# Kernel optimization log

Measured on AMD Instinct MI355X. Metric: run time of the kernel, lower is better.

Reference implementation:

```python
import jax, jax.numpy as jnp
import numpy as np

HEADS = 8
DIM_HEAD = 64
MAX_POS = 512
SCALE = DIM_HEAD ** -0.5

def setup_inputs() -> dict:
    key = jax.random.key(0)
    ks = jax.random.split(key, 4)
    b, n, dim = 32, 512, 512
    x = jax.random.normal(ks[0], (b, n, dim), dtype=jnp.float32)
    W_qkv = jax.random.normal(ks[1], (dim, 3 * HEADS * DIM_HEAD), dtype=jnp.float32) * (dim ** -0.5)
    rel_table = jax.random.normal(ks[2], (2 * MAX_POS + 1, DIM_HEAD), dtype=jnp.float32) * 0.02
    W_out = jax.random.normal(ks[3], (HEADS * DIM_HEAD, dim), dtype=jnp.float32) * ((HEADS * DIM_HEAD) ** -0.5)
    b_out = jnp.zeros((dim,), dtype=jnp.float32)
    return {"x": x, "W_qkv": W_qkv, "rel_table": rel_table, "W_out": W_out, "b_out": b_out}

def reference(x, W_qkv, rel_table, W_out, b_out):
    b, n, dim = x.shape
    qkv = x @ W_qkv  # [b, n, 3*h*d]
    q, k, v = jnp.split(qkv, 3, axis=-1)
    def heads(t):  # [b, n, h*d] -> [b, h, n, d]
        return t.reshape(b, n, HEADS, DIM_HEAD).transpose(0, 2, 1, 3)
    q, k, v = heads(q), heads(k), heads(v)
    dots = jnp.einsum('bhid,bhjd->bhij', q, k) * SCALE
    # relative position bias
    seq = jnp.arange(n)
    dist = jnp.clip(seq[:, None] - seq[None, :], -MAX_POS, MAX_POS) + MAX_POS  # [n, n]
    rel = rel_table[dist]  # [n, n(=r), d]
    pos_attn = jnp.einsum('bhnd,nrd->bhnr', q, rel) * SCALE
    dots = dots + pos_attn
    attn = jax.nn.softmax(dots.astype(jnp.float32), axis=-1).astype(q.dtype)
    out = jnp.einsum('bhij,bhjd->bhid', attn, v)  # [b, h, n, d]
    out = out.transpose(0, 2, 1, 3).reshape(b, n, HEADS * DIM_HEAD)
    return out @ W_out + b_out  # dropout=0.0 -> identity
```

## Files before the change

kernel.cpp:

```cpp
#include <hip/hip_runtime.h>

typedef __attribute__((ext_vector_type(8))) short short8;
typedef __attribute__((ext_vector_type(4))) float floatx4;

static constexpr size_t QOFF = 0;
static constexpr size_t KOFF = 8388608;
static constexpr size_t VTOFF = 16777216;
static constexpr size_t RBOFF = 25165824;
static constexpr size_t XBOFF = 25231424;
static constexpr size_t WTOFF = 33620032;
static constexpr size_t WOTOFF = 34406464;
static constexpr size_t OBOFF = 34668608;

__device__ inline unsigned short f2b(float f) {
  unsigned int u = __float_as_uint(f);
  u += 0x7fffu + ((u >> 16) & 1u);
  return (unsigned short)(u >> 16);
}
__device__ inline float b2f(unsigned short h) {
  return __uint_as_float(((unsigned int)h) << 16);
}

__global__ __launch_bounds__(256) void prep(const float* __restrict__ x,
                                            const float* __restrict__ Wqkv,
                                            const float* __restrict__ Wout,
                                            const float* __restrict__ rel,
                                            unsigned short* __restrict__ wsb) {
  __shared__ float T[64 * 65];
  const int bx = blockIdx.x;
  const int tid = threadIdx.x;
  if (bx < 4096) {
    size_t i8 = ((size_t)bx * 256 + tid) * 8;
    float4 a = *(const float4*)(x + i8);
    float4 b = *(const float4*)(x + i8 + 4);
    unsigned short t[8] = {f2b(a.x), f2b(a.y), f2b(a.z), f2b(a.w),
                           f2b(b.x), f2b(b.y), f2b(b.z), f2b(b.w)};
    *(uint4*)(wsb + XBOFF + i8) = *(uint4*)t;
  } else if (bx < 4352) {
    const bool isq = bx < 4288;
    const int z = isq ? bx - 4096 : bx - 4288;
    const int C = isq ? 1536 : 512;
    const int R = 512;
    const int c0 = (isq ? (z % 24) : (z % 8)) * 64;
    const int r0 = (isq ? (z / 24) : (z / 8)) * 64;
    const float* in = isq ? Wqkv : Wout;
    unsigned short* out = wsb + (isq ? WTOFF : WOTOFF);
#pragma unroll
    for (int p = 0; p < 4; ++p) {
      int r = (tid >> 4) + p * 16, c4 = (tid & 15) * 4;
      float4 v = *(const float4*)(in + (size_t)(r0 + r) * C + c0 + c4);
      T[r * 65 + c4 + 0] = v.x;
      T[r * 65 + c4 + 1] = v.y;
      T[r * 65 + c4 + 2] = v.z;
      T[r * 65 + c4 + 3] = v.w;
    }
    __syncthreads();
#pragma unroll
    for (int p = 0; p < 4; ++p) {
      int oc = (tid >> 4) + p * 16;
      int or4 = (tid & 15) * 4;
      unsigned short t[4];
#pragma unroll
      for (int j = 0; j < 4; ++j) t[j] = f2b(T[(or4 + j) * 65 + oc]);
      *(uint2*)(out + (size_t)(c0 + oc) * R + r0 + or4) = *(uint2*)t;
    }
  } else {
    int i = (bx - 4352) * 256 + tid;
    if (i < 65600) wsb[RBOFF + i] = f2b(rel[i]);
  }
}

__global__ __launch_bounds__(256) void qkv_mfma(const unsigned short* __restrict__ Xb,
                                                const unsigned short* __restrict__ Wt,
                                                unsigned short* __restrict__ wsb) {
  __shared__ __align__(16) unsigned short As[128 * 40];
  __shared__ __align__(16) unsigned short Bs[128 * 40];
  const int tid = threadIdx.x;
  const int w = tid >> 6, lane = tid & 63;
  const int g = lane >> 4, c = lane & 15;
  const int m0 = blockIdx.x * 128, n0 = blockIdx.y * 128;
  const int wr = (w >> 1) * 64, wc = (w & 1) * 64;
  const bool vmode = (blockIdx.y >= 8);

  const int rA = tid >> 2, oA = tid & 3;

  floatx4 acc[4][4];
#pragma unroll
  for (int mi = 0; mi < 4; ++mi)
#pragma unroll
    for (int ni = 0; ni < 4; ++ni) acc[mi][ni] = (floatx4){0.f, 0.f, 0.f, 0.f};

  uint4 pa0 = *(const uint4*)(Xb + (size_t)(m0 + rA) * 512 + oA * 8);
  uint4 pa1 = *(const uint4*)(Xb + (size_t)(m0 + rA + 64) * 512 + oA * 8);
  uint4 pb0 = *(const uint4*)(Wt + (size_t)(n0 + rA) * 512 + oA * 8);
  uint4 pb1 = *(const uint4*)(Wt + (size_t)(n0 + rA + 64) * 512 + oA * 8);

  for (int kk = 0; kk < 512; kk += 32) {
    __syncthreads();
    *(uint4*)(As + rA * 40 + oA * 8) = pa0;
    *(uint4*)(As + (rA + 64) * 40 + oA * 8) = pa1;
    *(uint4*)(Bs + rA * 40 + oA * 8) = pb0;
    *(uint4*)(Bs + (rA + 64) * 40 + oA * 8) = pb1;
    __syncthreads();
    const int kkn = (kk < 480) ? kk + 32 : kk;
    pa0 = *(const uint4*)(Xb + (size_t)(m0 + rA) * 512 + kkn + oA * 8);
    pa1 = *(const uint4*)(Xb + (size_t)(m0 + rA + 64) * 512 + kkn + oA * 8);
    pb0 = *(const uint4*)(Wt + (size_t)(n0 + rA) * 512 + kkn + oA * 8);
    pb1 = *(const uint4*)(Wt + (size_t)(n0 + rA + 64) * 512 + kkn + oA * 8);

    short8 a[4], b[4];
#pragma unroll
    for (int mi = 0; mi < 4; ++mi) a[mi] = *(const short8*)(As + (wr + mi * 16 + c) * 40 + g * 8);
#pragma unroll
    for (int ni = 0; ni < 4; ++ni) b[ni] = *(const short8*)(Bs + (wc + ni * 16 + c) * 40 + g * 8);
    if (vmode) {
#pragma unroll
      for (int mi = 0; mi < 4; ++mi)
#pragma unroll
        for (int ni = 0; ni < 4; ++ni)
          acc[mi][ni] = __builtin_amdgcn_mfma_f32_16x16x32_bf16(b[ni], a[mi], acc[mi][ni], 0, 0, 0);
    } else {
#pragma unroll
      for (int mi = 0; mi < 4; ++mi)
#pragma unroll
        for (int ni = 0; ni < 4; ++ni)
          acc[mi][ni] = __builtin_amdgcn_mfma_f32_16x16x32_bf16(a[mi], b[ni], acc[mi][ni], 0, 0, 0);
    }
  }

  constexpr float SCL = 0.125f * 1.44269504088896340736f;
  if (vmode) {
#pragma unroll
    for (int mi = 0; mi < 4; ++mi) {
      const int xrow = m0 + wr + mi * 16 + c;
      const int bb = xrow >> 9, nn = xrow & 511;
#pragma unroll
      for (int ni = 0; ni < 4; ++ni) {
#pragma unroll
        for (int r = 0; r < 4; ++r) {
          const int C = n0 + wc + ni * 16 + g * 4 + r;
          const int col512 = C & 511;
          const int h = col512 >> 6, d = col512 & 63;
          wsb[VTOFF + (size_t)(bb * 8 + h) * 32768 + (size_t)d * 512 + nn] = f2b(acc[mi][ni][r]);
        }
      }
    }
  } else {
    const size_t base = (blockIdx.y >= 4) ? KOFF : QOFF;
    const float scl = (blockIdx.y >= 4) ? 1.0f : SCL;
#pragma unroll
    for (int ni = 0; ni < 4; ++ni) {
      const int C = n0 + wc + ni * 16 + c;
      const int col512 = C & 511;
      const int h = col512 >> 6, d = col512 & 63;
#pragma unroll
      for (int mi = 0; mi < 4; ++mi) {
#pragma unroll
        for (int r = 0; r < 4; ++r) {
          const int xrow = m0 + wr + mi * 16 + g * 4 + r;
          wsb[base + (size_t)((xrow >> 9) * 8 + h) * 32768 + (size_t)(xrow & 511) * 64 + d] =
              f2b(acc[mi][ni][r] * scl);
        }
      }
    }
  }
}

__global__ __launch_bounds__(256) void attn_mfma(const unsigned short* __restrict__ wsb,
                                                 unsigned short* __restrict__ Ob) {
  __shared__ __align__(16) unsigned short Ks[64 * 72];
  __shared__ __align__(16) unsigned short Vt[64 * 72];
  __shared__ __align__(16) unsigned short Ps[64 * 72];
  __shared__ __align__(16) unsigned short Gs[4 * 16 * 84];

  const int tid = threadIdx.x;
  const int w = tid >> 6, lane = tid & 63;
  const int g = lane >> 4, c = lane & 15;
  const int i0 = blockIdx.x * 64, bh = blockIdx.y;

  const unsigned short* Qg = wsb + QOFF + (size_t)bh * 32768 + (size_t)i0 * 64;
  const unsigned short* Kg = wsb + KOFF + (size_t)bh * 32768;
  const unsigned short* Vg = wsb + VTOFF + (size_t)bh * 32768;
  const unsigned short* Rg = wsb + RBOFF;

  const short8 bq0 = *(const short8*)(Qg + (size_t)(w * 16 + c) * 64 + g * 8);
  const short8 bq1 = *(const short8*)(Qg + (size_t)(w * 16 + c) * 64 + 32 + g * 8);

  unsigned short* GsW = Gs + w * (16 * 84);
  unsigned short* PsW = Ps + (w * 16 + c) * 72;

  const int r0s = tid >> 3, o0s = tid & 7;
  const int r1s = r0s + 32;

  uint4 pk0 = *(const uint4*)(Kg + (size_t)r0s * 64 + o0s * 8);
  uint4 pk1 = *(const uint4*)(Kg + (size_t)r1s * 64 + o0s * 8);
  uint4 pv0 = *(const uint4*)(Vg + (size_t)r0s * 512 + o0s * 8);
  uint4 pv1 = *(const uint4*)(Vg + (size_t)r1s * 512 + o0s * 8);

  float m_i = -1e30f, l_i = 0.f;
  floatx4 oa[4];
#pragma unroll
  for (int t = 0; t < 4; ++t) oa[t] = (floatx4){0.f, 0.f, 0.f, 0.f};

  for (int jc = 0; jc < 8; ++jc) {
    const int j0 = jc * 64;
    __syncthreads();
    *(uint4*)(Ks + r0s * 72 + o0s * 8) = pk0;
    *(uint4*)(Ks + r1s * 72 + o0s * 8) = pk1;
    *(uint4*)(Vt + r0s * 72 + o0s * 8) = pv0;
    *(uint4*)(Vt + r1s * 72 + o0s * 8) = pv1;
    __syncthreads();

    const int dbase = i0 - j0 + 449 + w * 16;
    const unsigned short* Trow = Rg + (size_t)(dbase + c) * 64;
    short8 t0[5], t1[5];
#pragma unroll
    for (int dd = 0; dd < 5; ++dd) {
      t0[dd] = *(const short8*)(Trow + dd * 1024 + g * 8);
      t1[dd] = *(const short8*)(Trow + dd * 1024 + 32 + g * 8);
    }
    const int j0n = (jc < 7) ? j0 + 64 : j0;
    pk0 = *(const uint4*)(Kg + (size_t)(j0n + r0s) * 64 + o0s * 8);
    pk1 = *(const uint4*)(Kg + (size_t)(j0n + r1s) * 64 + o0s * 8);
    pv0 = *(const uint4*)(Vg + (size_t)r0s * 512 + j0n + o0s * 8);
    pv1 = *(const uint4*)(Vg + (size_t)r1s * 512 + j0n + o0s * 8);

    floatx4 s4[4];
#pragma unroll
    for (int t = 0; t < 4; ++t) {
      short8 k0 = *(const short8*)(Ks + (t * 16 + c) * 72 + g * 8);
      short8 k1 = *(const short8*)(Ks + (t * 16 + c) * 72 + 32 + g * 8);
      floatx4 sa = (floatx4){0.f, 0.f, 0.f, 0.f};
      sa = __builtin_amdgcn_mfma_f32_16x16x32_bf16(k0, bq0, sa, 0, 0, 0);
      sa = __builtin_amdgcn_mfma_f32_16x16x32_bf16(k1, bq1, sa, 0, 0, 0);
      s4[t] = sa;
    }

#pragma unroll
    for (int dd = 0; dd < 5; ++dd) {
      floatx4 ga = (floatx4){0.f, 0.f, 0.f, 0.f};
      ga = __builtin_amdgcn_mfma_f32_16x16x32_bf16(t0[dd], bq0, ga, 0, 0, 0);
      ga = __builtin_amdgcn_mfma_f32_16x16x32_bf16(t1[dd], bq1, ga, 0, 0, 0);
      unsigned short gk[4] = {f2b(ga[0]), f2b(ga[1]), f2b(ga[2]), f2b(ga[3])};
      *(uint2*)(GsW + c * 84 + dd * 16 + 4 * g) = *(uint2*)gk;
    }

    const unsigned short* Grow = GsW + c * 84 + c + 63;
#pragma unroll
    for (int t = 0; t < 4; ++t)
#pragma unroll
      for (int r = 0; r < 4; ++r) s4[t][r] += b2f(Grow[-(16 * t + 4 * g + r)]);

    float mx = -1e30f;
#pragma unroll
    for (int t = 0; t < 4; ++t)
      mx = fmaxf(mx, fmaxf(fmaxf(s4[t][0], s4[t][1]), fmaxf(s4[t][2], s4[t][3])));
    mx = fmaxf(mx, __shfl_xor(mx, 16));
    mx = fmaxf(mx, __shfl_xor(mx, 32));
    const float mn = fmaxf(m_i, mx);
    const float al = exp2f(m_i - mn);
    m_i = mn;
    float ls = 0.f;
#pragma unroll
    for (int t = 0; t < 4; ++t)
#pragma unroll
      for (int r = 0; r < 4; ++r) {
        float p = exp2f(s4[t][r] - mn);
        s4[t][r] = p;
        ls += p;
      }
    ls += __shfl_xor(ls, 16);
    ls += __shfl_xor(ls, 32);
    l_i = l_i * al + ls;

#pragma unroll
    for (int r = 0; r < 4; ++r) {
      const float ar = __shfl(al, 4 * g + r);
#pragma unroll
      for (int dt = 0; dt < 4; ++dt) oa[dt][r] *= ar;
    }

#pragma unroll
    for (int t = 0; t < 4; ++t) {
      unsigned short pk[4] = {f2b(s4[t][0]), f2b(s4[t][1]), f2b(s4[t][2]), f2b(s4[t][3])};
      *(uint2*)(PsW + t * 16 + 4 * g) = *(uint2*)pk;
    }

    short8 ap0 = *(const short8*)(PsW + g * 8);
    short8 ap1 = *(const short8*)(PsW + 32 + g * 8);
#pragma unroll
    for (int dt = 0; dt < 4; ++dt) {
      short8 bv0 = *(const short8*)(Vt + (dt * 16 + c) * 72 + g * 8);
      short8 bv1 = *(const short8*)(Vt + (dt * 16 + c) * 72 + 32 + g * 8);
      oa[dt] = __builtin_amdgcn_mfma_f32_16x16x32_bf16(ap0, bv0, oa[dt], 0, 0, 0);
      oa[dt] = __builtin_amdgcn_mfma_f32_16x16x32_bf16(ap1, bv1, oa[dt], 0, 0, 0);
    }
  }

  const int b = bh >> 3, h = bh & 7;
  const float invl = 1.0f / l_i;
#pragma unroll
  for (int r = 0; r < 4; ++r) {
    const float inv = __shfl(invl, 4 * g + r);
    const int i = i0 + w * 16 + 4 * g + r;
    const size_t rowoff = ((size_t)(b * 512 + i)) * 512 + h * 64;
#pragma unroll
    for (int dt = 0; dt < 4; ++dt) Ob[rowoff + dt * 16 + c] = f2b(oa[dt][r] * inv);
  }
}

__global__ __launch_bounds__(256) void out_mfma(const unsigned short* __restrict__ Ab,
                                                const unsigned short* __restrict__ Bt,
                                                const float* __restrict__ bias,
                                                float* __restrict__ out) {
  __shared__ __align__(16) unsigned short As[128 * 40];
  __shared__ __align__(16) unsigned short Bs[128 * 40];
  const int tid = threadIdx.x;
  const int w = tid >> 6, lane = tid & 63;
  const int g = lane >> 4, c = lane & 15;
  const int m0 = blockIdx.x * 128, n0 = blockIdx.y * 128;
  const int wr = (w >> 1) * 64, wc = (w & 1) * 64;

  floatx4 acc[4][4];
#pragma unroll
  for (int mi = 0; mi < 4; ++mi)
#pragma unroll
    for (int ni = 0; ni < 4; ++ni) acc[mi][ni] = (floatx4){0.f, 0.f, 0.f, 0.f};

  for (int kk = 0; kk < 512; kk += 32) {
    __syncthreads();
#pragma unroll
    for (int p = 0; p < 2; ++p) {
      int e = tid + 256 * p;
      int r = e >> 2, o = e & 3;
      *(uint4*)(As + r * 40 + o * 8) = *(const uint4*)(Ab + (size_t)(m0 + r) * 512 + kk + o * 8);
      *(uint4*)(Bs + r * 40 + o * 8) = *(const uint4*)(Bt + (size_t)(n0 + r) * 512 + kk + o * 8);
    }
    __syncthreads();
    short8 a[4], b[4];
#pragma unroll
    for (int mi = 0; mi < 4; ++mi) a[mi] = *(const short8*)(As + (wr + mi * 16 + c) * 40 + g * 8);
#pragma unroll
    for (int ni = 0; ni < 4; ++ni) b[ni] = *(const short8*)(Bs + (wc + ni * 16 + c) * 40 + g * 8);
#pragma unroll
    for (int mi = 0; mi < 4; ++mi)
#pragma unroll
      for (int ni = 0; ni < 4; ++ni)
        acc[mi][ni] = __builtin_amdgcn_mfma_f32_16x16x32_bf16(a[mi], b[ni], acc[mi][ni], 0, 0, 0);
  }

#pragma unroll
  for (int ni = 0; ni < 4; ++ni) {
    const int C = n0 + wc + ni * 16 + c;
    const float bv = bias[C];
#pragma unroll
    for (int mi = 0; mi < 4; ++mi) {
#pragma unroll
      for (int r = 0; r < 4; ++r) {
        const int m = m0 + wr + mi * 16 + g * 4 + r;
        out[(size_t)m * 512 + C] = acc[mi][ni][r] + bv;
      }
    }
  }
}

extern "C" void kernel_launch(void* const* d_in, const int* in_sizes, int n_in,
                              void* d_out, int out_size, void* d_ws, size_t ws_size,
                              hipStream_t stream) {
  const float* x = (const float*)d_in[0];
  const float* Wqkv = (const float*)d_in[1];
  const float* rel = (const float*)d_in[2];
  const float* Wout = (const float*)d_in[3];
  const float* bout = (const float*)d_in[4];
  float* out = (float*)d_out;
  unsigned short* wsb = (unsigned short*)d_ws;

  prep<<<4609, 256, 0, stream>>>(x, Wqkv, Wout, rel, wsb);
  qkv_mfma<<<dim3(128, 12), 256, 0, stream>>>(wsb + XBOFF, wsb + WTOFF, wsb);
  attn_mfma<<<dim3(8, 256), 256, 0, stream>>>(wsb, wsb + OBOFF);
  out_mfma<<<dim3(128, 4), 256, 0, stream>>>(wsb + OBOFF, wsb + WOTOFF, bout, out);
}
```

Baseline: 247.0 us.

## Cheapen bf16 packing, merge attention LDS buffers, reorder grid, prefetch out GEMM tiles

```diff
diff --git a/kernel.cpp b/kernel.cpp
--- a/kernel.cpp
+++ b/kernel.cpp
@@ -13,12 +13,14 @@
 static constexpr size_t OBOFF = 34668608;
 
 __device__ inline unsigned short f2b(float f) {
-  unsigned int u = __float_as_uint(f);
-  u += 0x7fffu + ((u >> 16) & 1u);
-  return (unsigned short)(u >> 16);
+  return (unsigned short)((__float_as_uint(f) + 0x8000u) >> 16);
 }
 __device__ inline float b2f(unsigned short h) {
   return __uint_as_float(((unsigned int)h) << 16);
+}
+__device__ inline unsigned int pk2(float hi, float lo) {
+  return __builtin_amdgcn_perm(__float_as_uint(hi) + 0x8000u,
+                               __float_as_uint(lo) + 0x8000u, 0x07060302u);
 }
 
 __global__ __launch_bounds__(256) void prep(const float* __restrict__ x,
@@ -33,9 +35,8 @@
     size_t i8 = ((size_t)bx * 256 + tid) * 8;
     float4 a = *(const float4*)(x + i8);
     float4 b = *(const float4*)(x + i8 + 4);
-    unsigned short t[8] = {f2b(a.x), f2b(a.y), f2b(a.z), f2b(a.w),
-                           f2b(b.x), f2b(b.y), f2b(b.z), f2b(b.w)};
-    *(uint4*)(wsb + XBOFF + i8) = *(uint4*)t;
+    uint4 o = {pk2(a.y, a.x), pk2(a.w, a.z), pk2(b.y, b.x), pk2(b.w, b.z)};
+    *(uint4*)(wsb + XBOFF + i8) = o;
   } else if (bx < 4352) {
     const bool isq = bx < 4288;
     const int z = isq ? bx - 4096 : bx - 4288;
@@ -59,10 +60,9 @@
     for (int p = 0; p < 4; ++p) {
       int oc = (tid >> 4) + p * 16;
       int or4 = (tid & 15) * 4;
-      unsigned short t[4];
-#pragma unroll
-      for (int j = 0; j < 4; ++j) t[j] = f2b(T[(or4 + j) * 65 + oc]);
-      *(uint2*)(out + (size_t)(c0 + oc) * R + r0 + or4) = *(uint2*)t;
+      uint2 o = {pk2(T[(or4 + 1) * 65 + oc], T[(or4 + 0) * 65 + oc]),
+                 pk2(T[(or4 + 3) * 65 + oc], T[(or4 + 2) * 65 + oc])};
+      *(uint2*)(out + (size_t)(c0 + oc) * R + r0 + or4) = o;
     }
   } else {
     int i = (bx - 4352) * 256 + tid;
@@ -170,13 +170,12 @@
                                                  unsigned short* __restrict__ Ob) {
   __shared__ __align__(16) unsigned short Ks[64 * 72];
   __shared__ __align__(16) unsigned short Vt[64 * 72];
-  __shared__ __align__(16) unsigned short Ps[64 * 72];
-  __shared__ __align__(16) unsigned short Gs[4 * 16 * 84];
+  __shared__ __align__(16) unsigned short U[4 * 16 * 88];
 
   const int tid = threadIdx.x;
   const int w = tid >> 6, lane = tid & 63;
   const int g = lane >> 4, c = lane & 15;
-  const int i0 = blockIdx.x * 64, bh = blockIdx.y;
+  const int bh = blockIdx.x, i0 = blockIdx.y * 64;
 
   const unsigned short* Qg = wsb + QOFF + (size_t)bh * 32768 + (size_t)i0 * 64;
   const unsigned short* Kg = wsb + KOFF + (size_t)bh * 32768;
@@ -186,8 +185,8 @@
   const short8 bq0 = *(const short8*)(Qg + (size_t)(w * 16 + c) * 64 + g * 8);
   const short8 bq1 = *(const short8*)(Qg + (size_t)(w * 16 + c) * 64 + 32 + g * 8);
 
-  unsigned short* GsW = Gs + w * (16 * 84);
-  unsigned short* PsW = Ps + (w * 16 + c) * 72;
+  unsigned short* UW = U + w * (16 * 88);
+  unsigned short* RowW = UW + c * 88;
 
   const int r0s = tid >> 3, o0s = tid & 7;
   const int r1s = r0s + 32;
@@ -241,11 +240,11 @@
       floatx4 ga = (floatx4){0.f, 0.f, 0.f, 0.f};
       ga = __builtin_amdgcn_mfma_f32_16x16x32_bf16(t0[dd], bq0, ga, 0, 0, 0);
       ga = __builtin_amdgcn_mfma_f32_16x16x32_bf16(t1[dd], bq1, ga, 0, 0, 0);
-      unsigned short gk[4] = {f2b(ga[0]), f2b(ga[1]), f2b(ga[2]), f2b(ga[3])};
-      *(uint2*)(GsW + c * 84 + dd * 16 + 4 * g) = *(uint2*)gk;
-    }
-
-    const unsigned short* Grow = GsW + c * 84 + c + 63;
+      uint2 gk = {pk2(ga[1], ga[0]), pk2(ga[3], ga[2])};
+      *(uint2*)(RowW + dd * 16 + 4 * g) = gk;
+    }
+
+    const unsigned short* Grow = RowW + c + 63;
 #pragma unroll
     for (int t = 0; t < 4; ++t)
 #pragma unroll
@@ -282,12 +281,12 @@
 
 #pragma unroll
     for (int t = 0; t < 4; ++t) {
-      unsigned short pk[4] = {f2b(s4[t][0]), f2b(s4[t][1]), f2b(s4[t][2]), f2b(s4[t][3])};
-      *(uint2*)(PsW + t * 16 + 4 * g) = *(uint2*)pk;
-    }
-
-    short8 ap0 = *(const short8*)(PsW + g * 8);
-    short8 ap1 = *(const short8*)(PsW + 32 + g * 8);
+      uint2 pk = {pk2(s4[t][1], s4[t][0]), pk2(s4[t][3], s4[t][2])};
+      *(uint2*)(RowW + t * 16 + 4 * g) = pk;
+    }
+
+    short8 ap0 = *(const short8*)(RowW + g * 8);
+    short8 ap1 = *(const short8*)(RowW + 32 + g * 8);
 #pragma unroll
     for (int dt = 0; dt < 4; ++dt) {
       short8 bv0 = *(const short8*)(Vt + (dt * 16 + c) * 72 + g * 8);
@@ -321,22 +320,32 @@
   const int m0 = blockIdx.x * 128, n0 = blockIdx.y * 128;
   const int wr = (w >> 1) * 64, wc = (w & 1) * 64;
 
+  const int rA = tid >> 2, oA = tid & 3;
+
   floatx4 acc[4][4];
 #pragma unroll
   for (int mi = 0; mi < 4; ++mi)
 #pragma unroll
     for (int ni = 0; ni < 4; ++ni) acc[mi][ni] = (floatx4){0.f, 0.f, 0.f, 0.f};
 
+  uint4 pa0 = *(const uint4*)(Ab + (size_t)(m0 + rA) * 512 + oA * 8);
+  uint4 pa1 = *(const uint4*)(Ab + (size_t)(m0 + rA + 64) * 512 + oA * 8);
+  uint4 pb0 = *(const uint4*)(Bt + (size_t)(n0 + rA) * 512 + oA * 8);
+  uint4 pb1 = *(const uint4*)(Bt + (size_t)(n0 + rA + 64) * 512 + oA * 8);
+
   for (int kk = 0; kk < 512; kk += 32) {
     __syncthreads();
-#pragma unroll
-    for (int p = 0; p < 2; ++p) {
-      int e = tid + 256 * p;
-      int r = e >> 2, o = e & 3;
-      *(uint4*)(As + r * 40 + o * 8) = *(const uint4*)(Ab + (size_t)(m0 + r) * 512 + kk + o * 8);
-      *(uint4*)(Bs + r * 40 + o * 8) = *(const uint4*)(Bt + (size_t)(n0 + r) * 512 + kk + o * 8);
-    }
-    __syncthreads();
+    *(uint4*)(As + rA * 40 + oA * 8) = pa0;
+    *(uint4*)(As + (rA + 64) * 40 + oA * 8) = pa1;
+    *(uint4*)(Bs + rA * 40 + oA * 8) = pb0;
+    *(uint4*)(Bs + (rA + 64) * 40 + oA * 8) = pb1;
+    __syncthreads();
+    const int kkn = (kk < 480) ? kk + 32 : kk;
+    pa0 = *(const uint4*)(Ab + (size_t)(m0 + rA) * 512 + kkn + oA * 8);
+    pa1 = *(const uint4*)(Ab + (size_t)(m0 + rA + 64) * 512 + kkn + oA * 8);
+    pb0 = *(const uint4*)(Bt + (size_t)(n0 + rA) * 512 + kkn + oA * 8);
+    pb1 = *(const uint4*)(Bt + (size_t)(n0 + rA + 64) * 512 + kkn + oA * 8);
+
     short8 a[4], b[4];
 #pragma unroll
     for (int mi = 0; mi < 4; ++mi) a[mi] = *(const short8*)(As + (wr + mi * 16 + c) * 40 + g * 8);
@@ -377,6 +386,6 @@
 
   prep<<<4609, 256, 0, stream>>>(x, Wqkv, Wout, rel, wsb);
   qkv_mfma<<<dim3(128, 12), 256, 0, stream>>>(wsb + XBOFF, wsb + WTOFF, wsb);
-  attn_mfma<<<dim3(8, 256), 256, 0, stream>>>(wsb, wsb + OBOFF);
+  attn_mfma<<<dim3(256, 8), 256, 0, stream>>>(wsb, wsb + OBOFF);
   out_mfma<<<dim3(128, 4), 256, 0, stream>>>(wsb + OBOFF, wsb + WOTOFF, bout, out);
 }
```

New measurement: 262.0 us. +6.1%, slower.
